# Kernel tuning notes

Measured on AMD Instinct MI355X. Metric: run time of the kernel, lower is better.

The kernel has to match this reference:

```python
import jax, jax.numpy as jnp
import numpy as np

N_IMG, N_CAP, N_RGN, MAX_W, EMBED = 32, 32, 36, 50, 1024
LAMBDA_SOFTMAX = 9.0
NORM_EPS = 1e-12  # F.normalize default eps


def setup_inputs() -> dict:
    key = jax.random.key(0)
    ks = jax.random.split(key, 13)
    rgn = jax.random.normal(ks[0], (N_IMG, N_RGN, EMBED), jnp.float32)
    img = jax.random.normal(ks[1], (N_IMG, EMBED), jnp.float32)
    wrd = jax.random.normal(ks[2], (N_CAP, MAX_W, EMBED), jnp.float32)
    stc = jax.random.normal(ks[3], (N_CAP, EMBED), jnp.float32)
    # ragged caption lengths in [1, MAX_W]
    stc_lens = jax.random.randint(ks[4], (N_CAP,), 1, MAX_W + 1, dtype=jnp.int32)
    s = 1.0 / np.sqrt(EMBED)
    w_scale = jax.random.normal(ks[5], (EMBED, EMBED), jnp.float32) * s
    b_scale = jnp.zeros((EMBED,), jnp.float32)
    w_shift = jax.random.normal(ks[6], (EMBED, EMBED), jnp.float32) * s
    b_shift = jnp.zeros((EMBED,), jnp.float32)
    w1 = jax.random.normal(ks[7], (EMBED, EMBED), jnp.float32) * s
    b1 = jnp.zeros((EMBED,), jnp.float32)
    w2 = jax.random.normal(ks[8], (EMBED, EMBED), jnp.float32) * s
    b2 = jnp.zeros((EMBED,), jnp.float32)
    return dict(rgn=rgn, img=img, wrd=wrd, stc=stc, stc_lens=stc_lens,
                w_scale=w_scale, b_scale=b_scale, w_shift=w_shift, b_shift=b_shift,
                w1=w1, b1=b1, w2=w2, b2=b2)


def reference(rgn, img, wrd, stc, stc_lens, w_scale, b_scale, w_shift, b_shift, w1, b1, w2, b2):
    # rgn: (I, Q, D) regions; wrd: (C, L, D) ragged words; stc_lens: (C,)
    C, L, D = wrd.shape
    valid = jnp.arange(L)[None, :] < stc_lens[:, None]          # (C, L)
    # scores[c,i,l,q] = wrd[c,l] . rgn[i,q]  (bmm(context, queryT))
    s = jnp.einsum('cld,iqd->cilq', wrd, rgn)                   # (C, I, L, Q)
    s = jnp.where(s >= 0, s, 0.1 * s)                           # LeakyReLU(0.1)
    # L2-normalize over the query (region) axis, per (c,i,l)
    s = s / jnp.maximum(jnp.sqrt(jnp.sum(s * s, axis=3, keepdims=True)), NORM_EPS)
    # temperature softmax over valid words (ragged mask)
    logits = jnp.where(valid[:, None, :, None], s * LAMBDA_SOFTMAX, -jnp.inf)
    attn = jax.nn.softmax(logits, axis=2)                       # (C, I, L, Q)
    # weightedContext[c,i,q,d] = sum_l attn * wrd
    wei = jnp.einsum('cilq,cld->ciqd', attn, wrd)               # (C, I, Q, D)
    # FiLM-style refine
    scaling = jnp.tanh(jnp.einsum('ciqd,ed->ciqe', wei, w_scale) + b_scale)
    shifting = jnp.einsum('ciqd,ed->ciqe', wei, w_shift) + b_shift
    x = rgn[None] * scaling + shifting                          # (C, I, Q, D)
    h = jax.nn.relu(jnp.einsum('ciqd,ed->ciqe', x, w1) + b1)
    modu = jnp.einsum('ciqd,ed->ciqe', h, w2) + b2
    ref = modu + rgn[None]
    # torch cats per-caption results along dim=1 -> (I, C, Q, D)
    return jnp.transpose(ref, (1, 0, 2, 3))
```

## Files before the change

### kernel.cpp

```cpp
#include <hip/hip_runtime.h>
#include <math.h>

#define NC 32
#define NI 32
#define NL 50
#define NQ 36
#define ND 1024
#define LAMBDA 9.0f

#define BM 128
#define BN 128

typedef __attribute__((ext_vector_type(8))) short bf16x8;
typedef __attribute__((ext_vector_type(4))) float floatx4;

static __device__ __forceinline__ unsigned short f2b(float f) {
    unsigned int u = __float_as_uint(f);
    unsigned int r = (u + 0x7fffu + ((u >> 16) & 1u)) >> 16;
    return (unsigned short)r;
}
static __device__ __forceinline__ float bf2f(unsigned short u) {
    return __uint_as_float(((unsigned int)u) << 16);
}

static __device__ __forceinline__ float ftanh(float x) {
    float ax = fabsf(x);
    float e = __expf(ax + ax);
    return copysignf(1.f - 2.f / (e + 1.f), x);
}

static __device__ __forceinline__ void gload16(const unsigned short* g, unsigned short* l) {
    __builtin_amdgcn_global_load_lds(
        (const __attribute__((address_space(1))) unsigned int*)g,
        (__attribute__((address_space(3))) unsigned int*)l, 16, 0, 0);
}

struct CvtJob { const float* src; unsigned short* dst; int n2; int valid2; };
struct CvtJobs { CvtJob j[5]; };

__global__ __launch_bounds__(256) void k_cvt(CvtJobs jobs) {
    CvtJob jb = jobs.j[blockIdx.y];
    unsigned int* d32 = (unsigned int*)jb.dst;
    int stride = gridDim.x * 256;
    for (int i = blockIdx.x * 256 + threadIdx.x; i < jb.n2; i += stride) {
        unsigned int pk = 0;
        if (i < jb.valid2) {
            float2 v = ((const float2*)jb.src)[i];
            pk = (unsigned int)f2b(v.x) | ((unsigned int)f2b(v.y) << 16);
        }
        d32[i] = pk;
    }
}

struct HlJob { const float* src; unsigned short* hi; unsigned short* lo; int n2; };
struct HlJobs { HlJob j[2]; };

__global__ __launch_bounds__(256) void k_cvt_hilo(HlJobs jobs) {
    HlJob jb = jobs.j[blockIdx.y];
    unsigned int* h32 = (unsigned int*)jb.hi;
    unsigned int* l32 = (unsigned int*)jb.lo;
    int stride = gridDim.x * 256;
    for (int i = blockIdx.x * 256 + threadIdx.x; i < jb.n2; i += stride) {
        float2 v = ((const float2*)jb.src)[i];
        unsigned short h0 = f2b(v.x), h1 = f2b(v.y);
        unsigned short l0 = f2b(v.x - bf2f(h0)), l1 = f2b(v.y - bf2f(h1));
        h32[i] = (unsigned int)h0 | ((unsigned int)h1 << 16);
        l32[i] = (unsigned int)l0 | ((unsigned int)l1 << 16);
    }
}

#define SST 37

__global__ __launch_bounds__(256) void k_attn(
    const unsigned short* __restrict__ whi, const unsigned short* __restrict__ wlo,
    const unsigned short* __restrict__ rhi, const unsigned short* __restrict__ rlo,
    const int* __restrict__ lens, unsigned short* __restrict__ attn)
{
    int bx = blockIdx.x;
    int c = bx / NI, i = bx % NI;
    __shared__ __align__(16) unsigned short Wh[64 * 32], Wl[64 * 32];
    __shared__ __align__(16) unsigned short Rh[48 * 32], Rl[48 * 32];
    __shared__ float S[64 * SST];
    int t = threadIdx.x, lane = t & 63, wid = t >> 6;
    int lrow = lane & 15, quad = lane >> 4;
    int len = lens[c];

    int grow = lane >> 2;
    int ssw = ((lane & 3) ^ ((lane >> 3) & 3)) * 8;
    const unsigned short* garr = (wid == 0) ? whi : (wid == 1) ? wlo : (wid == 2) ? rhi : rlo;
    unsigned short* larr = (wid == 0) ? Wh : (wid == 1) ? Wl : (wid == 2) ? Rh : Rl;
    int ngroups = (wid < 2) ? 4 : 3;
    size_t gbase = (wid < 2) ? (size_t)(c * NL) * ND : (size_t)(i * NQ) * ND;

    floatx4 acc[3] = {};
    int fsw = (quad ^ ((lrow >> 1) & 3)) * 8;

    for (int kt = 0; kt < ND; kt += 32) {
        for (int j = 0; j < ngroups; ++j) {
            int row = j * 16 + grow;
            gload16(garr + gbase + (size_t)row * ND + kt + ssw, larr + j * 512 + lane * 8);
        }
        __syncthreads();
        bf16x8 ah = *(const bf16x8*)&Wh[(wid * 16 + lrow) * 32 + fsw];
        bf16x8 al = *(const bf16x8*)&Wl[(wid * 16 + lrow) * 32 + fsw];
#pragma unroll
        for (int nt = 0; nt < 3; ++nt) {
            bf16x8 bh = *(const bf16x8*)&Rh[(nt * 16 + lrow) * 32 + fsw];
            bf16x8 bl = *(const bf16x8*)&Rl[(nt * 16 + lrow) * 32 + fsw];
            acc[nt] = __builtin_amdgcn_mfma_f32_16x16x32_bf16(ah, bh, acc[nt], 0, 0, 0);
            acc[nt] = __builtin_amdgcn_mfma_f32_16x16x32_bf16(ah, bl, acc[nt], 0, 0, 0);
            acc[nt] = __builtin_amdgcn_mfma_f32_16x16x32_bf16(al, bh, acc[nt], 0, 0, 0);
        }
        __syncthreads();
    }
#pragma unroll
    for (int nt = 0; nt < 3; ++nt) {
        int q = nt * 16 + lrow;
        if (q < NQ) {
#pragma unroll
            for (int r = 0; r < 4; ++r) {
                int l = wid * 16 + quad * 4 + r;
                S[l * SST + q] = acc[nt][r];
            }
        }
    }
    __syncthreads();
    if (t < 200) {
        int l = t >> 2, part = t & 3;
        float lv[9];
        float ss = 0.f;
#pragma unroll
        for (int jj = 0; jj < 9; ++jj) {
            int q = part * 9 + jj;
            float v = S[l * SST + q];
            float x = (v >= 0.f) ? v : 0.1f * v;
            lv[jj] = x;
            ss += x * x;
        }
        ss += __shfl_xor(ss, 1);
        ss += __shfl_xor(ss, 2);
        float inv = LAMBDA / fmaxf(sqrtf(ss), 1e-12f);
#pragma unroll
        for (int jj = 0; jj < 9; ++jj) S[l * SST + part * 9 + jj] = lv[jj] * inv;
    }
    __syncthreads();
    if (t < 144) {
        int q = t >> 2, part = t & 3;
        int ls = part * 13;
        int le = ls + 13 < len ? ls + 13 : len;
        float m = -1e30f;
        for (int l = ls; l < le; ++l) m = fmaxf(m, S[l * SST + q]);
        m = fmaxf(m, __shfl_xor(m, 1));
        m = fmaxf(m, __shfl_xor(m, 2));
        float sum = 0.f;
        for (int l = ls; l < le; ++l) sum += __expf(S[l * SST + q] - m);
        sum += __shfl_xor(sum, 1);
        sum += __shfl_xor(sum, 2);
        float inv = 1.f / sum;
        unsigned int* o = (unsigned int*)attn + ((size_t)(c * NI + i) * NQ + q) * 32;
        int jb = part * 8;
#pragma unroll
        for (int jj = 0; jj < 8; ++jj) {
            int j = jb + jj;
            int l0 = 2 * j, l1 = 2 * j + 1;
            unsigned short a0 = (l0 < len) ? f2b(__expf(S[l0 * SST + q] - m) * inv) : (unsigned short)0;
            unsigned short a1 = (l1 < len) ? f2b(__expf(S[l1 * SST + q] - m) * inv) : (unsigned short)0;
            o[j] = (unsigned int)a0 | ((unsigned int)a1 << 16);
        }
    }
}

__global__ __launch_bounds__(256, 2) void k_pgemm(
    const unsigned short* __restrict__ A, const unsigned short* __restrict__ B1,
    const unsigned short* __restrict__ B2, unsigned short* __restrict__ P1,
    unsigned short* __restrict__ P2)
{
    const int K = ND;
    const int BK = 32;
    int bn = blockIdx.x, bm = blockIdx.y;
    const unsigned short* B = blockIdx.z ? B2 : B1;
    unsigned short* P = blockIdx.z ? P2 : P1;
    int m0 = bm * BM, n0 = bn * BN;

    __shared__ __align__(16) unsigned short At[BM * 32];
    __shared__ __align__(16) unsigned short Bt[BN * 32];

    int t = threadIdx.x, lane = t & 63, wid = t >> 6;
    int wx = wid & 1, wy = wid >> 1;
    int lrow = lane & 15, quad = lane >> 4;
    floatx4 acc[4][4] = {};

    int srow = t >> 2, pos = t & 3;
    int ssw = (pos ^ ((srow >> 1) & 3)) * 8;
    const unsigned short* Aptr = A + (size_t)(m0 + srow) * K + ssw;
    const unsigned short* Bptr = B + (size_t)(n0 + srow) * K + ssw;
    unsigned short* Al  = &At[srow * BK + pos * 8];
    unsigned short* Al2 = &At[(srow + 64) * BK + pos * 8];
    unsigned short* Bl  = &Bt[srow * BK + pos * 8];
    unsigned short* Bl2 = &Bt[(srow + 64) * BK + pos * 8];
    int fsw = (quad ^ ((lrow >> 1) & 3)) * 8;

    for (int kt = 0; kt < K; kt += BK) {
        gload16(Aptr + kt, Al);
        gload16(Aptr + (size_t)64 * K + kt, Al2);
        gload16(Bptr + kt, Bl);
        gload16(Bptr + (size_t)64 * K + kt, Bl2);
        __syncthreads();
        bf16x8 af[4], bfr[4];
#pragma unroll
        for (int im = 0; im < 4; ++im)
            af[im] = *(const bf16x8*)&At[(wy * 64 + im * 16 + lrow) * BK + fsw];
#pragma unroll
        for (int in = 0; in < 4; ++in)
            bfr[in] = *(const bf16x8*)&Bt[(wx * 64 + in * 16 + lrow) * BK + fsw];
#pragma unroll
        for (int im = 0; im < 4; ++im)
#pragma unroll
            for (int in = 0; in < 4; ++in)
                acc[im][in] = __builtin_amdgcn_mfma_f32_16x16x32_bf16(
                    af[im], bfr[in], acc[im][in], 0, 0, 0);
        __syncthreads();
    }
#pragma unroll
    for (int im = 0; im < 4; ++im)
#pragma unroll
        for (int in = 0; in < 4; ++in) {
            int n = n0 + wx * 64 + in * 16 + lrow;
#pragma unroll
            for (int r = 0; r < 4; ++r) {
                int m = m0 + wy * 64 + im * 16 + quad * 4 + r;
                int c = m / NL, l = m - c * NL;
                if (c < NC) P[((size_t)(c * ND + n)) * 64 + l] = f2b(acc[im][in][r]);
            }
        }
}

__global__ __launch_bounds__(256, 2) void k_attn_gemm(
    const unsigned short* __restrict__ attn, const unsigned short* __restrict__ Psc,
    const unsigned short* __restrict__ Psh, const float* __restrict__ bsc,
    const float* __restrict__ bsh, const float* __restrict__ rgnf,
    unsigned short* __restrict__ xbuf)
{
    int bn = blockIdx.x, bm = blockIdx.y, c = blockIdx.z;
    __shared__ __align__(16) unsigned short smem3[3 * 128 * 64];
    unsigned short* At  = smem3;
    unsigned short* B1t = smem3 + 8192;
    unsigned short* B2t = smem3 + 16384;
    unsigned short* Ct  = smem3;
    int t = threadIdx.x, lane = t & 63, wid = t >> 6;
    int wx = wid & 1, wy = wid >> 1;
    int lrow = lane & 15, quad = lane >> 4;
    int grow = lane >> 3, pos = lane & 7;

    const unsigned short* Ab  = attn + (size_t)(c * 1152 + bm * 128) * 64;
    const unsigned short* B1b = Psc + (size_t)(c * ND + bn * 128) * 64;
    const unsigned short* B2b = Psh + (size_t)(c * ND + bn * 128) * 64;
    for (int g = wid; g < 16; g += 4) {
        int row = g * 8 + grow;
        int ssw = (pos ^ (row & 7)) * 8;
        gload16(Ab + (size_t)row * 64 + ssw, &At[g * 512 + lane * 8]);
        gload16(B1b + (size_t)row * 64 + ssw, &B1t[g * 512 + lane * 8]);
        gload16(B2b + (size_t)row * 64 + ssw, &B2t[g * 512 + lane * 8]);
    }
    __syncthreads();

    floatx4 acc[4][4] = {}, acc2[4][4] = {};
#pragma unroll
    for (int kk = 0; kk < 2; ++kk) {
        int sw = ((kk * 4 + quad) ^ (lrow & 7)) * 8;
        bf16x8 af[4], b1f[4], b2f[4];
#pragma unroll
        for (int im = 0; im < 4; ++im)
            af[im] = *(const bf16x8*)&At[(wy * 64 + im * 16 + lrow) * 64 + sw];
#pragma unroll
        for (int in = 0; in < 4; ++in) {
            b1f[in] = *(const bf16x8*)&B1t[(wx * 64 + in * 16 + lrow) * 64 + sw];
            b2f[in] = *(const bf16x8*)&B2t[(wx * 64 + in * 16 + lrow) * 64 + sw];
        }
#pragma unroll
        for (int im = 0; im < 4; ++im)
#pragma unroll
            for (int in = 0; in < 4; ++in) {
                acc[im][in] = __builtin_amdgcn_mfma_f32_16x16x32_bf16(
                    af[im], b1f[in], acc[im][in], 0, 0, 0);
                acc2[im][in] = __builtin_amdgcn_mfma_f32_16x16x32_bf16(
                    af[im], b2f[in], acc2[im][in], 0, 0, 0);
            }
    }
    __syncthreads();
#pragma unroll
    for (int im = 0; im < 4; ++im)
#pragma unroll
        for (int in = 0; in < 4; ++in) {
            int n = bn * 128 + wx * 64 + in * 16 + lrow;
            float b1v = bsc[n], b2v = bsh[n];
#pragma unroll
            for (int r = 0; r < 4; ++r) {
                int row = wy * 64 + im * 16 + quad * 4 + r;
                int m = bm * 128 + row;
                int i = m / NQ, q = m - i * NQ;
                float sc = ftanh(acc[im][in][r] + b1v);
                float sh = acc2[im][in][r] + b2v;
                float rg = rgnf[(size_t)(i * NQ + q) * ND + n];
                int colc = (wx * 8 + in * 2 + (lrow >> 3)) ^ (row & 7);
                Ct[row * 128 + colc * 8 + (lrow & 7)] = f2b(rg * sc + sh);
            }
        }
    __syncthreads();
#pragma unroll
    for (int p = 0; p < 8; ++p) {
        int row = p * 16 + (t >> 4), chunk = t & 15;
        int m = bm * 128 + row;
        int i = m / NQ, q = m - i * NQ;
        size_t dr = ((size_t)(i * NC + c) * NQ + q) * ND + bn * 128 + chunk * 8;
        *(bf16x8*)&xbuf[dr] = *(const bf16x8*)&Ct[row * 128 + ((chunk ^ (row & 7)) * 8)];
    }
}

template <int MODE, int MINW>
__global__ __launch_bounds__(256, MINW) void k_gemm(
    const unsigned short* __restrict__ A, const unsigned short* __restrict__ B1,
    const float* __restrict__ bias1, const float* __restrict__ rgnf,
    void* __restrict__ outp)
{
    const int K = ND;
    int lin = blockIdx.x;
    int xcd = lin & 7;
    int kb = lin >> 3;
    int bm = xcd * 36 + (kb >> 3);
    int bn = kb & 7;
    int m0 = bm * BM, n0 = bn * BN;

    __shared__ __align__(16) unsigned short smem[2 * 128 * 64];
    unsigned short* At = smem;
    unsigned short* Bt = smem + 8192;
    unsigned short* Ct = smem;

    int t = threadIdx.x;
    int lane = t & 63, wid = t >> 6;
    int wx = wid & 1, wy = wid >> 1;
    int lrow = lane & 15, quad = lane >> 4;

    floatx4 acc[4][4] = {};

    int srow = t >> 3, pos = t & 7;
    int ssw = (pos ^ (srow & 7)) * 8;
    const unsigned short* Aptr  = A  + (size_t)(m0 + srow) * K + ssw;
    const unsigned short* B1ptr = B1 + (size_t)(n0 + srow) * K + ssw;
    unsigned short* ldA = At + t * 8;
    unsigned short* ldB = Bt + t * 8;

    for (int kt = 0; kt < K; kt += 64) {
#pragma unroll
        for (int p = 0; p < 4; ++p) {
            gload16(Aptr + (size_t)(p * 32) * K + kt, ldA + p * 2048);
            gload16(B1ptr + (size_t)(p * 32) * K + kt, ldB + p * 2048);
        }
        __syncthreads();
#pragma unroll
        for (int kh = 0; kh < 2; ++kh) {
            int sw = ((kh * 4 + quad) ^ (lrow & 7)) * 8;
            bf16x8 af[4], bfr[4];
#pragma unroll
            for (int im = 0; im < 4; ++im)
                af[im] = *(const bf16x8*)&At[(wy * 64 + im * 16 + lrow) * 64 + sw];
#pragma unroll
            for (int in = 0; in < 4; ++in)
                bfr[in] = *(const bf16x8*)&Bt[(wx * 64 + in * 16 + lrow) * 64 + sw];
#pragma unroll
            for (int im = 0; im < 4; ++im)
#pragma unroll
                for (int in = 0; in < 4; ++in)
                    acc[im][in] = __builtin_amdgcn_mfma_f32_16x16x32_bf16(
                        af[im], bfr[in], acc[im][in], 0, 0, 0);
        }
        __syncthreads();
    }

    if constexpr (MODE == 1) {
#pragma unroll
        for (int im = 0; im < 4; ++im)
#pragma unroll
            for (int in = 0; in < 4; ++in) {
                int n = n0 + wx * 64 + in * 16 + lrow;
                float b1v = bias1[n];
#pragma unroll
                for (int r = 0; r < 4; ++r) {
                    int row = wy * 64 + im * 16 + quad * 4 + r;
                    float h = acc[im][in][r] + b1v;
                    h = h > 0.f ? h : 0.f;
                    int colc = (wx * 8 + in * 2 + (lrow >> 3)) ^ (row & 7);
                    Ct[row * 128 + colc * 8 + (lrow & 7)] = f2b(h);
                }
            }
        __syncthreads();
        unsigned short* ob = (unsigned short*)outp + (size_t)m0 * ND + n0;
#pragma unroll
        for (int p = 0; p < 8; ++p) {
            int row = p * 16 + (t >> 4), chunk = t & 15;
            *(bf16x8*)&ob[(size_t)row * ND + chunk * 8] =
                *(const bf16x8*)&Ct[row * 128 + ((chunk ^ (row & 7)) * 8)];
        }
    } else {
#pragma unroll
        for (int im = 0; im < 4; ++im)
#pragma unroll
            for (int in = 0; in < 4; ++in) {
                int n = n0 + wx * 64 + in * 16 + lrow;
                float b1v = bias1[n];
#pragma unroll
                for (int r = 0; r < 4; ++r) {
                    int m = m0 + wy * 64 + im * 16 + quad * 4 + r;
                    int i = m / (NC * NQ);
                    int q = m % NQ;
                    float rg = rgnf[(size_t)(i * NQ + q) * ND + n];
                    ((float*)outp)[(size_t)m * ND + n] = acc[im][in][r] + b1v + rg;
                }
            }
    }
}

extern "C" void kernel_launch(void* const* d_in, const int* in_sizes, int n_in,
                              void* d_out, int out_size, void* d_ws, size_t ws_size,
                              hipStream_t stream) {
    const float* rgn     = (const float*)d_in[0];
    const float* wrd     = (const float*)d_in[2];
    const int*   lens    = (const int*)d_in[4];
    const float* w_scale = (const float*)d_in[5];
    const float* b_scale = (const float*)d_in[6];
    const float* w_shift = (const float*)d_in[7];
    const float* b_shift = (const float*)d_in[8];
    const float* w1      = (const float*)d_in[9];
    const float* b1      = (const float*)d_in[10];
    const float* w2      = (const float*)d_in[11];
    const float* b2      = (const float*)d_in[12];
    float* outf = (float*)d_out;

    char* ws = (char*)d_ws;
    unsigned short* wsc_bf = (unsigned short*)(ws + 0);
    unsigned short* wsh_bf = (unsigned short*)(ws + 2097152);
    unsigned short* w1_bf  = (unsigned short*)(ws + 4194304);
    unsigned short* w2_bf  = (unsigned short*)(ws + 6291456);
    unsigned short* wrd_bf = (unsigned short*)(ws + 8388608);
    unsigned short* attn   = (unsigned short*)(ws + 11796480);
    unsigned short* P_sct  = (unsigned short*)(ws + 16515072);
    unsigned short* P_sht  = (unsigned short*)(ws + 20709376);
    unsigned short* wrd_hi = (unsigned short*)(ws + 24903680);
    unsigned short* wrd_lo = (unsigned short*)(ws + 28209152);
    unsigned short* rgn_hi = (unsigned short*)(ws + 31514624);
    unsigned short* rgn_lo = (unsigned short*)(ws + 33898496);
    unsigned short* hbuf   = (unsigned short*)(ws + 8388608);
    unsigned short* xbuf   = (unsigned short*)d_out;

    CvtJobs jobs;
    jobs.j[0] = { w_scale, wsc_bf, ND * ND / 2, ND * ND / 2 };
    jobs.j[1] = { w_shift, wsh_bf, ND * ND / 2, ND * ND / 2 };
    jobs.j[2] = { w1,      w1_bf,  ND * ND / 2, ND * ND / 2 };
    jobs.j[3] = { w2,      w2_bf,  ND * ND / 2, ND * ND / 2 };
    jobs.j[4] = { wrd,     wrd_bf, 1664 * ND / 2, NC * NL * ND / 2 };
    k_cvt<<<dim3(128, 5), 256, 0, stream>>>(jobs);

    HlJobs hjobs;
    hjobs.j[0] = { wrd, wrd_hi, wrd_lo, NC * NL * ND / 2 };
    hjobs.j[1] = { rgn, rgn_hi, rgn_lo, NI * NQ * ND / 2 };
    k_cvt_hilo<<<dim3(128, 2), 256, 0, stream>>>(hjobs);

    k_attn<<<NC * NI, 256, 0, stream>>>(wrd_hi, wrd_lo, rgn_hi, rgn_lo, lens, attn);

    k_pgemm<<<dim3(8, 13, 2), 256, 0, stream>>>(wrd_bf, wsc_bf, wsh_bf, P_sct, P_sht);

    k_attn_gemm<<<dim3(8, 9, 32), 256, 0, stream>>>(attn, P_sct, P_sht,
                                                    b_scale, b_shift, rgn, xbuf);

    k_gemm<1, 2><<<2304, 256, 0, stream>>>(xbuf, w1_bf, b1, rgn, hbuf);
    k_gemm<2, 2><<<2304, 256, 0, stream>>>(hbuf, w2_bf, b2, rgn, outf);
}
```

Baseline: 435.5 us.

## Double-buffer LDS tiles in attention and GEMM kernels; fuse scale/shift projection GEMMs

The attention-score kernel, the projection GEMM and the two main MLP GEMMs now use two LDS buffers. The next K-tile is loaded while the current one is consumed, which removes one barrier per iteration and lets global loads overlap with MFMA work. The projection GEMM also computes both the scale and shift products in one block, so the shared A tile is loaded once instead of twice. The cost is doubled LDS use: the main GEMMs move to 64KB of dynamic shared memory, and the fused GEMM carries twice the accumulators, which raises register pressure and may lower occupancy.

```diff
diff --git a/kernel.cpp b/kernel.cpp
--- a/kernel.cpp
+++ b/kernel.cpp
@@ -70,6 +70,7 @@
 }
 
 #define SST 37
+#define KVB 7168
 
 __global__ __launch_bounds__(256) void k_attn(
     const unsigned short* __restrict__ whi, const unsigned short* __restrict__ wlo,
@@ -78,8 +79,7 @@
 {
     int bx = blockIdx.x;
     int c = bx / NI, i = bx % NI;
-    __shared__ __align__(16) unsigned short Wh[64 * 32], Wl[64 * 32];
-    __shared__ __align__(16) unsigned short Rh[48 * 32], Rl[48 * 32];
+    __shared__ __align__(16) unsigned short KV[2][KVB];
     __shared__ float S[64 * SST];
     int t = threadIdx.x, lane = t & 63, wid = t >> 6;
     int lrow = lane & 15, quad = lane >> 4;
@@ -88,25 +88,36 @@
     int grow = lane >> 2;
     int ssw = ((lane & 3) ^ ((lane >> 3) & 3)) * 8;
     const unsigned short* garr = (wid == 0) ? whi : (wid == 1) ? wlo : (wid == 2) ? rhi : rlo;
-    unsigned short* larr = (wid == 0) ? Wh : (wid == 1) ? Wl : (wid == 2) ? Rh : Rl;
+    const int aoffs[4] = { 0, 2048, 4096, 5632 };
+    int aoff = aoffs[wid];
     int ngroups = (wid < 2) ? 4 : 3;
     size_t gbase = (wid < 2) ? (size_t)(c * NL) * ND : (size_t)(i * NQ) * ND;
 
     floatx4 acc[3] = {};
     int fsw = (quad ^ ((lrow >> 1) & 3)) * 8;
 
+    for (int j = 0; j < ngroups; ++j) {
+        int row = j * 16 + grow;
+        gload16(garr + gbase + (size_t)row * ND + ssw, &KV[0][aoff + j * 512 + lane * 8]);
+    }
+    __syncthreads();
+
     for (int kt = 0; kt < ND; kt += 32) {
-        for (int j = 0; j < ngroups; ++j) {
-            int row = j * 16 + grow;
-            gload16(garr + gbase + (size_t)row * ND + kt + ssw, larr + j * 512 + lane * 8);
-        }
-        __syncthreads();
-        bf16x8 ah = *(const bf16x8*)&Wh[(wid * 16 + lrow) * 32 + fsw];
-        bf16x8 al = *(const bf16x8*)&Wl[(wid * 16 + lrow) * 32 + fsw];
+        int cb = (kt >> 5) & 1;
+        if (kt + 32 < ND) {
+            for (int j = 0; j < ngroups; ++j) {
+                int row = j * 16 + grow;
+                gload16(garr + gbase + (size_t)row * ND + (kt + 32) + ssw,
+                        &KV[cb ^ 1][aoff + j * 512 + lane * 8]);
+            }
+        }
+        const unsigned short* KVc = KV[cb];
+        bf16x8 ah = *(const bf16x8*)&KVc[(wid * 16 + lrow) * 32 + fsw];
+        bf16x8 al = *(const bf16x8*)&KVc[2048 + (wid * 16 + lrow) * 32 + fsw];
 #pragma unroll
         for (int nt = 0; nt < 3; ++nt) {
-            bf16x8 bh = *(const bf16x8*)&Rh[(nt * 16 + lrow) * 32 + fsw];
-            bf16x8 bl = *(const bf16x8*)&Rl[(nt * 16 + lrow) * 32 + fsw];
+            bf16x8 bh = *(const bf16x8*)&KVc[4096 + (nt * 16 + lrow) * 32 + fsw];
+            bf16x8 bl = *(const bf16x8*)&KVc[5632 + (nt * 16 + lrow) * 32 + fsw];
             acc[nt] = __builtin_amdgcn_mfma_f32_16x16x32_bf16(ah, bh, acc[nt], 0, 0, 0);
             acc[nt] = __builtin_amdgcn_mfma_f32_16x16x32_bf16(ah, bl, acc[nt], 0, 0, 0);
             acc[nt] = __builtin_amdgcn_mfma_f32_16x16x32_bf16(al, bh, acc[nt], 0, 0, 0);
@@ -170,7 +181,7 @@
     }
 }
 
-__global__ __launch_bounds__(256, 2) void k_pgemm(
+__global__ __launch_bounds__(256) void k_pgemm(
     const unsigned short* __restrict__ A, const unsigned short* __restrict__ B1,
     const unsigned short* __restrict__ B2, unsigned short* __restrict__ P1,
     unsigned short* __restrict__ P2)
@@ -178,49 +189,62 @@
     const int K = ND;
     const int BK = 32;
     int bn = blockIdx.x, bm = blockIdx.y;
-    const unsigned short* B = blockIdx.z ? B2 : B1;
-    unsigned short* P = blockIdx.z ? P2 : P1;
     int m0 = bm * BM, n0 = bn * BN;
 
-    __shared__ __align__(16) unsigned short At[BM * 32];
-    __shared__ __align__(16) unsigned short Bt[BN * 32];
+    __shared__ __align__(16) unsigned short smem[2][3 * 4096];
 
     int t = threadIdx.x, lane = t & 63, wid = t >> 6;
     int wx = wid & 1, wy = wid >> 1;
     int lrow = lane & 15, quad = lane >> 4;
-    floatx4 acc[4][4] = {};
+    floatx4 acc1[4][4] = {}, acc2[4][4] = {};
 
     int srow = t >> 2, pos = t & 3;
     int ssw = (pos ^ ((srow >> 1) & 3)) * 8;
-    const unsigned short* Aptr = A + (size_t)(m0 + srow) * K + ssw;
-    const unsigned short* Bptr = B + (size_t)(n0 + srow) * K + ssw;
-    unsigned short* Al  = &At[srow * BK + pos * 8];
-    unsigned short* Al2 = &At[(srow + 64) * BK + pos * 8];
-    unsigned short* Bl  = &Bt[srow * BK + pos * 8];
-    unsigned short* Bl2 = &Bt[(srow + 64) * BK + pos * 8];
+    const unsigned short* Aptr  = A  + (size_t)(m0 + srow) * K + ssw;
+    const unsigned short* B1ptr = B1 + (size_t)(n0 + srow) * K + ssw;
+    const unsigned short* B2ptr = B2 + (size_t)(n0 + srow) * K + ssw;
+    int dst0 = srow * BK + pos * 8;
     int fsw = (quad ^ ((lrow >> 1) & 3)) * 8;
 
+#define PG_STAGE(b, kt) { \
+    unsigned short* s0 = smem[b]; \
+    gload16(Aptr + (kt), &s0[dst0]); \
+    gload16(Aptr + (size_t)64 * K + (kt), &s0[dst0 + 2048]); \
+    gload16(B1ptr + (kt), &s0[4096 + dst0]); \
+    gload16(B1ptr + (size_t)64 * K + (kt), &s0[4096 + dst0 + 2048]); \
+    gload16(B2ptr + (kt), &s0[8192 + dst0]); \
+    gload16(B2ptr + (size_t)64 * K + (kt), &s0[8192 + dst0 + 2048]); }
+
+    PG_STAGE(0, 0)
+    __syncthreads();
+
     for (int kt = 0; kt < K; kt += BK) {
-        gload16(Aptr + kt, Al);
-        gload16(Aptr + (size_t)64 * K + kt, Al2);
-        gload16(Bptr + kt, Bl);
-        gload16(Bptr + (size_t)64 * K + kt, Bl2);
-        __syncthreads();
-        bf16x8 af[4], bfr[4];
+        int cb = (kt >> 5) & 1;
+        if (kt + BK < K) PG_STAGE(cb ^ 1, kt + BK)
+        const unsigned short* At  = smem[cb];
+        const unsigned short* Bt1 = smem[cb] + 4096;
+        const unsigned short* Bt2 = smem[cb] + 8192;
+        bf16x8 af[4], b1f[4], b2f[4];
 #pragma unroll
         for (int im = 0; im < 4; ++im)
             af[im] = *(const bf16x8*)&At[(wy * 64 + im * 16 + lrow) * BK + fsw];
 #pragma unroll
-        for (int in = 0; in < 4; ++in)
-            bfr[in] = *(const bf16x8*)&Bt[(wx * 64 + in * 16 + lrow) * BK + fsw];
+        for (int in = 0; in < 4; ++in) {
+            b1f[in] = *(const bf16x8*)&Bt1[(wx * 64 + in * 16 + lrow) * BK + fsw];
+            b2f[in] = *(const bf16x8*)&Bt2[(wx * 64 + in * 16 + lrow) * BK + fsw];
+        }
 #pragma unroll
         for (int im = 0; im < 4; ++im)
 #pragma unroll
-            for (int in = 0; in < 4; ++in)
-                acc[im][in] = __builtin_amdgcn_mfma_f32_16x16x32_bf16(
-                    af[im], bfr[in], acc[im][in], 0, 0, 0);
+            for (int in = 0; in < 4; ++in) {
+                acc1[im][in] = __builtin_amdgcn_mfma_f32_16x16x32_bf16(
+                    af[im], b1f[in], acc1[im][in], 0, 0, 0);
+                acc2[im][in] = __builtin_amdgcn_mfma_f32_16x16x32_bf16(
+                    af[im], b2f[in], acc2[im][in], 0, 0, 0);
+            }
         __syncthreads();
     }
+#undef PG_STAGE
 #pragma unroll
     for (int im = 0; im < 4; ++im)
 #pragma unroll
@@ -230,7 +254,10 @@
             for (int r = 0; r < 4; ++r) {
                 int m = m0 + wy * 64 + im * 16 + quad * 4 + r;
                 int c = m / NL, l = m - c * NL;
-                if (c < NC) P[((size_t)(c * ND + n)) * 64 + l] = f2b(acc[im][in][r]);
+                if (c < NC) {
+                    P1[((size_t)(c * ND + n)) * 64 + l] = f2b(acc1[im][in][r]);
+                    P2[((size_t)(c * ND + n)) * 64 + l] = f2b(acc2[im][in][r]);
+                }
             }
         }
 }
@@ -324,6 +351,9 @@
     void* __restrict__ outp)
 {
     const int K = ND;
+    extern __shared__ unsigned short smem[];
+    unsigned short* Ct = smem;
+
     int lin = blockIdx.x;
     int xcd = lin & 7;
     int kb = lin >> 3;
@@ -331,11 +361,6 @@
     int bn = kb & 7;
     int m0 = bm * BM, n0 = bn * BN;
 
-    __shared__ __align__(16) unsigned short smem[2 * 128 * 64];
-    unsigned short* At = smem;
-    unsigned short* Bt = smem + 8192;
-    unsigned short* Ct = smem;
-
     int t = threadIdx.x;
     int lane = t & 63, wid = t >> 6;
     int wx = wid & 1, wy = wid >> 1;
@@ -347,16 +372,23 @@
     int ssw = (pos ^ (srow & 7)) * 8;
     const unsigned short* Aptr  = A  + (size_t)(m0 + srow) * K + ssw;
     const unsigned short* B1ptr = B1 + (size_t)(n0 + srow) * K + ssw;
-    unsigned short* ldA = At + t * 8;
-    unsigned short* ldB = Bt + t * 8;
+
+#define G_STAGE(b, kt) { \
+    unsigned short* dA = smem + (b) * 16384 + t * 8; \
+    unsigned short* dB = smem + (b) * 16384 + 8192 + t * 8; \
+    _Pragma("unroll") \
+    for (int p = 0; p < 4; ++p) { \
+        gload16(Aptr + (size_t)(p * 32) * K + (kt), dA + p * 2048); \
+        gload16(B1ptr + (size_t)(p * 32) * K + (kt), dB + p * 2048); } }
+
+    G_STAGE(0, 0)
+    __syncthreads();
 
     for (int kt = 0; kt < K; kt += 64) {
-#pragma unroll
-        for (int p = 0; p < 4; ++p) {
-            gload16(Aptr + (size_t)(p * 32) * K + kt, ldA + p * 2048);
-            gload16(B1ptr + (size_t)(p * 32) * K + kt, ldB + p * 2048);
-        }
-        __syncthreads();
+        int cb = (kt >> 6) & 1;
+        if (kt + 64 < K) G_STAGE(cb ^ 1, kt + 64)
+        const unsigned short* At = smem + cb * 16384;
+        const unsigned short* Bt = At + 8192;
 #pragma unroll
         for (int kh = 0; kh < 2; ++kh) {
             int sw = ((kh * 4 + quad) ^ (lrow & 7)) * 8;
@@ -376,6 +408,7 @@
         }
         __syncthreads();
     }
+#undef G_STAGE
 
     if constexpr (MODE == 1) {
 #pragma unroll
@@ -452,6 +485,15 @@
     unsigned short* hbuf   = (unsigned short*)(ws + 8388608);
     unsigned short* xbuf   = (unsigned short*)d_out;
 
+    static int s_attr = []() {
+        hipFuncSetAttribute((const void*)k_gemm<1, 2>,
+                            hipFuncAttributeMaxDynamicSharedMemorySize, 65536);
+        hipFuncSetAttribute((const void*)k_gemm<2, 2>,
+                            hipFuncAttributeMaxDynamicSharedMemorySize, 65536);
+        return 0;
+    }();
+    (void)s_attr;
+
     CvtJobs jobs;
     jobs.j[0] = { w_scale, wsc_bf, ND * ND / 2, ND * ND / 2 };
     jobs.j[1] = { w_shift, wsh_bf, ND * ND / 2, ND * ND / 2 };
@@ -467,11 +509,11 @@
 
     k_attn<<<NC * NI, 256, 0, stream>>>(wrd_hi, wrd_lo, rgn_hi, rgn_lo, lens, attn);
 
-    k_pgemm<<<dim3(8, 13, 2), 256, 0, stream>>>(wrd_bf, wsc_bf, wsh_bf, P_sct, P_sht);
+    k_pgemm<<<dim3(8, 13), 256, 0, stream>>>(wrd_bf, wsc_bf, wsh_bf, P_sct, P_sht);
 
     k_attn_gemm<<<dim3(8, 9, 32), 256, 0, stream>>>(attn, P_sct, P_sht,
                                                     b_scale, b_shift, rgn, xbuf);
 
-    k_gemm<1, 2><<<2304, 256, 0, stream>>>(xbuf, w1_bf, b1, rgn, hbuf);
-    k_gemm<2, 2><<<2304, 256, 0, stream>>>(hbuf, w2_bf, b2, rgn, outf);
-}
+    k_gemm<1, 2><<<2304, 256, 65536, stream>>>(xbuf, w1_bf, b1, rgn, hbuf);
+    k_gemm<2, 2><<<2304, 256, 65536, stream>>>(hbuf, w2_bf, b2, rgn, outf);
+}
```

New measurement: 495.7 us. +13.8%, slower.
